# Kernel optimization log

Measured on AMD Instinct MI355X. Metric: run time of the kernel, lower is better.

Reference implementation:

```python
import jax, jax.numpy as jnp
import numpy as np

B, L, E, D = 4, 4096, 768, 64

def setup_inputs() -> dict:
    key = jax.random.key(0)
    ks = jax.random.split(key, 7)
    x = jax.random.normal(ks[0], (B, L, E), dtype=jnp.float32)
    # True = masked (strict upper triangle), as in masked_fill semantics
    causal_mask = jnp.triu(jnp.ones((L, L), dtype=bool), k=1)
    # True = valid token (inverted with ~ inside forward); all valid to avoid NaN rows
    pad_mask = jnp.ones((B, L), dtype=bool)
    s = 1.0 / np.sqrt(E)
    Wk = jax.random.uniform(ks[1], (E, D), jnp.float32, -s, s)
    bk = jax.random.uniform(ks[2], (D,), jnp.float32, -s, s)
    Wq = jax.random.uniform(ks[3], (E, D), jnp.float32, -s, s)
    bq = jax.random.uniform(ks[4], (D,), jnp.float32, -s, s)
    Wv = jax.random.uniform(ks[5], (E, D), jnp.float32, -s, s)
    bv = jax.random.uniform(ks[6], (D,), jnp.float32, -s, s)
    return {"x": x, "causal_mask": causal_mask, "pad_mask": pad_mask,
            "Wk": Wk, "bk": bk, "Wq": Wq, "bq": bq, "Wv": Wv, "bv": bv}

def reference(x, causal_mask, pad_mask, Wk, bk, Wq, bq, Wv, bv):
    # Linear projections: [B,L,E] @ [E,D] + [D]
    K = jnp.einsum('ble,ed->bld', x, Wk) + bk
    Q = jnp.einsum('ble,ed->bld', x, Wq) + bq
    V = jnp.einsum('ble,ed->bld', x, Wv) + bv
    d = Q.shape[-1]
    scores = jnp.einsum('bqd,bkd->bqk', Q, K) / jnp.sqrt(jnp.asarray(d, Q.dtype))
    # full_mask: causal (True=masked) OR key-position padding (~pad_mask, broadcast over query dim)
    full_mask = causal_mask[None, :, :] | (~pad_mask)[:, None, :]
    scores = jnp.where(full_mask, -jnp.inf, scores)
    attn = jax.nn.softmax(scores, axis=-1)
    out = jnp.einsum('bqk,bkd->bqd', attn, V)
    return out
```

## Files before the change

kernel.cpp:

```cpp
#include <hip/hip_runtime.h>

#define L_SEQ 4096
#define BATCH 4
#define EDIM 768

typedef __attribute__((ext_vector_type(8))) short bf16x8;
typedef __attribute__((ext_vector_type(4))) float f32x4;
typedef __attribute__((ext_vector_type(4))) unsigned short u16x4;
typedef __attribute__((ext_vector_type(8))) unsigned short u16x8;
typedef __attribute__((ext_vector_type(4))) _Float16 f16x4;
typedef __attribute__((ext_vector_type(8))) _Float16 f16x8;

__device__ __forceinline__ unsigned short f2bf(float f) {
  unsigned u = __builtin_bit_cast(unsigned, f);
  u += 0x7FFFu + ((u >> 16) & 1u);
  return (unsigned short)(u >> 16);
}

__global__ __launch_bounds__(256) void prep_kernel(
    const float* __restrict__ Wq, const float* __restrict__ Wk,
    const float* __restrict__ Wv, unsigned short* __restrict__ WT) {
  int g = blockIdx.x * 256 + threadIdx.x;
  if (g >= 192 * EDIM) return;
  int row = g / EDIM, k = g - row * EDIM;
  int z = row >> 6, n = row & 63;
  const float* W = (z == 0) ? Wq : (z == 1) ? Wk : Wv;
  WT[g] = f2bf(W[k * 64 + n]);
}

__global__ __launch_bounds__(256) void proj_kernel(
    const float* __restrict__ x, const unsigned short* __restrict__ WT,
    const float* __restrict__ bq, const float* __restrict__ bk, const float* __restrict__ bv,
    unsigned short* __restrict__ Qo, unsigned short* __restrict__ Kf,
    _Float16* __restrict__ Vf) {
  __shared__ unsigned short As[64 * 72];
  __shared__ unsigned short Bs[192 * 72];
  int tid = threadIdx.x;
  int w = tid >> 6, lane = tid & 63, l15 = lane & 15, g4 = lane >> 4;
  int m0 = blockIdx.x * 64;

  f32x4 acc[3][4];
#pragma unroll
  for (int z = 0; z < 3; z++)
#pragma unroll
    for (int cf = 0; cf < 4; cf++) acc[z][cf] = (f32x4){0.f, 0.f, 0.f, 0.f};

  int arow = tid >> 4, acs = tid & 15;
  int brow = tid >> 3, bsg = tid & 7;

  for (int k0 = 0; k0 < EDIM; k0 += 64) {
#pragma unroll
    for (int p = 0; p < 4; p++) {
      int row = arow + p * 16;
      f32x4 v = *(const f32x4*)(x + (size_t)(m0 + row) * EDIM + k0 + acs * 4);
      u16x4 sv;
      sv[0] = f2bf(v[0]); sv[1] = f2bf(v[1]); sv[2] = f2bf(v[2]); sv[3] = f2bf(v[3]);
      *(u16x4*)(&As[row * 72 + acs * 4]) = sv;
    }
#pragma unroll
    for (int p = 0; p < 6; p++) {
      int row = brow + p * 32;
      u16x8 v = *(const u16x8*)(WT + (size_t)row * EDIM + k0 + bsg * 8);
      *(u16x8*)(&Bs[row * 72 + bsg * 8]) = v;
    }
    __syncthreads();
#pragma unroll
    for (int ks = 0; ks < 64; ks += 32) {
      bf16x8 a = *(const bf16x8*)(&As[(16 * w + l15) * 72 + ks + g4 * 8]);
#pragma unroll
      for (int z = 0; z < 3; z++) {
#pragma unroll
        for (int cf = 0; cf < 4; cf++) {
          bf16x8 bb = *(const bf16x8*)(&Bs[(z * 64 + cf * 16 + l15) * 72 + ks + g4 * 8]);
          acc[z][cf] = __builtin_amdgcn_mfma_f32_16x16x32_bf16(a, bb, acc[z][cf], 0, 0, 0);
        }
      }
    }
    __syncthreads();
  }

#pragma unroll
  for (int cf = 0; cf < 4; cf++) {
    int col = cf * 16 + l15;
    float bqv = bq[col], bkv = bk[col], bvv = bv[col];
#pragma unroll
    for (int r = 0; r < 4; r++) {
      int row = m0 + 16 * w + g4 * 4 + r;
      Qo[(size_t)row * 64 + col] = f2bf((acc[0][cf][r] + bqv) * 0.125f);
      int b_ = row >> 12, l = row & 4095, j = l >> 6, t = l & 63;
      size_t blk = (size_t)(b_ * 64 + j) * 4096;
      size_t kidx = blk + (size_t)(((col >> 5) * 4 + (t >> 4)) * 512 +
                                   (((col >> 3) & 3) * 16 + (t & 15)) * 8 + (col & 7));
      Kf[kidx] = f2bf(acc[1][cf][r] + bkv);
      size_t vidx = blk + (size_t)(((t >> 4) * 2 + (col >> 5)) * 512 +
                                   ((((t >> 2) & 3) * 16) + (col & 15)) * 8 +
                                   ((col >> 4) & 1) * 4 + (t & 3));
      Vf[vidx] = (_Float16)(acc[2][cf][r] + bvv);
    }
  }
}

__global__ __launch_bounds__(256) void attn_kernel(
    const unsigned short* __restrict__ Qp, const unsigned short* __restrict__ Kf,
    const _Float16* __restrict__ Vf, float* __restrict__ out) {
  __shared__ float Ob[2][4][16][68];
  __shared__ float Ml[2][4][2][16];
  int tid = threadIdx.x;
  int p = tid >> 6, lane = tid & 63, l15 = lane & 15, g4 = lane >> 4;
  int flat = blockIdx.x;
  int xcd = flat & 7;
  int b = xcd >> 1;
  int pid = ((xcd & 1) << 6) + (flat >> 3);
  int sA = pid, sB = 255 - pid;
  size_t bL = (size_t)b * L_SEQ;

  float mA, lA; f32x4 oA[4];
  float mB, lB; f32x4 oB[4];

  auto run = [&](int s, f32x4 (&o)[4], float& m, float& l) {
    m = -1e38f; l = 0.f;
#pragma unroll
    for (int i = 0; i < 4; i++) o[i] = (f32x4){0.f, 0.f, 0.f, 0.f};
    int qrow = s * 16 + l15;
    const unsigned short* Qb = Qp + (bL + qrow) * 64 + g4 * 8;
    bf16x8 qf0 = *(const bf16x8*)Qb;
    bf16x8 qf1 = *(const bf16x8*)(Qb + 32);
    int jmax = s >> 2;
    for (int j = p; j <= jmax; j += 4) {
      const unsigned short* kb = Kf + (size_t)(b * 64 + j) * 4096 + lane * 8;
      const _Float16* vb = Vf + (size_t)(b * 64 + j) * 4096 + lane * 8;
      bf16x8 kf0[4], kf1[4];
#pragma unroll
      for (int tb = 0; tb < 4; tb++) kf0[tb] = *(const bf16x8*)(kb + tb * 512);
#pragma unroll
      for (int tb = 0; tb < 4; tb++) kf1[tb] = *(const bf16x8*)(kb + 2048 + tb * 512);
      f16x8 vp[8];
#pragma unroll
      for (int q = 0; q < 8; q++) vp[q] = *(const f16x8*)(vb + q * 512);

      f32x4 st[4];
#pragma unroll
      for (int tb = 0; tb < 4; tb++) st[tb] = (f32x4){0.f, 0.f, 0.f, 0.f};
#pragma unroll
      for (int tb = 0; tb < 4; tb++)
        st[tb] = __builtin_amdgcn_mfma_f32_16x16x32_bf16(kf0[tb], qf0, st[tb], 0, 0, 0);
#pragma unroll
      for (int tb = 0; tb < 4; tb++)
        st[tb] = __builtin_amdgcn_mfma_f32_16x16x32_bf16(kf1[tb], qf1, st[tb], 0, 0, 0);

      if (j == jmax) {
#pragma unroll
        for (int tb = 0; tb < 4; tb++)
#pragma unroll
          for (int r = 0; r < 4; r++)
            if (j * 64 + tb * 16 + g4 * 4 + r > qrow) st[tb][r] = -1e30f;
      }

      float mx = st[0][0];
#pragma unroll
      for (int tb = 0; tb < 4; tb++)
#pragma unroll
        for (int r = 0; r < 4; r++) mx = fmaxf(mx, st[tb][r]);
      mx = fmaxf(mx, __shfl_xor(mx, 16));
      mx = fmaxf(mx, __shfl_xor(mx, 32));
      float mn = fmaxf(m, mx);
      float scale = __expf(m - mn);
      m = mn;
      float rs = 0.f;
#pragma unroll
      for (int tb = 0; tb < 4; tb++)
#pragma unroll
        for (int r = 0; r < 4; r++) { st[tb][r] = __expf(st[tb][r] - mn); rs += st[tb][r]; }
      rs += __shfl_xor(rs, 16);
      rs += __shfl_xor(rs, 32);
      l = l * scale + rs;
#pragma unroll
      for (int cf = 0; cf < 4; cf++)
#pragma unroll
        for (int r = 0; r < 4; r++) o[cf][r] *= scale;

      f16x4 ph[4];
#pragma unroll
      for (int tb = 0; tb < 4; tb++) {
        ph[tb][0] = (_Float16)st[tb][0];
        ph[tb][1] = (_Float16)st[tb][1];
        ph[tb][2] = (_Float16)st[tb][2];
        ph[tb][3] = (_Float16)st[tb][3];
      }
#pragma unroll
      for (int tb = 0; tb < 4; tb++) {
#pragma unroll
        for (int cf = 0; cf < 4; cf++) {
          f16x8 pr = vp[tb * 2 + (cf >> 1)];
          f16x4 va = (cf & 1) ? (f16x4){pr[4], pr[5], pr[6], pr[7]}
                              : (f16x4){pr[0], pr[1], pr[2], pr[3]};
          o[cf] = __builtin_amdgcn_mfma_f32_16x16x16f16(va, ph[tb], o[cf], 0, 0, 0);
        }
      }
    }
  };

  run(sA, oA, mA, lA);
  run(sB, oB, mB, lB);

#pragma unroll
  for (int cf = 0; cf < 4; cf++) {
    *(f32x4*)&Ob[0][p][l15][cf * 16 + g4 * 4] = oA[cf];
    *(f32x4*)&Ob[1][p][l15][cf * 16 + g4 * 4] = oB[cf];
  }
  Ml[0][p][0][l15] = mA; Ml[0][p][1][l15] = lA;
  Ml[1][p][0][l15] = mB; Ml[1][p][1][l15] = lB;
  __syncthreads();

  if (p < 2) {
    int s = p ? sB : sA;
    int q = lane >> 2, ch = lane & 3;
    float mw[4], lw[4];
#pragma unroll
    for (int w = 0; w < 4; w++) { mw[w] = Ml[p][w][0][q]; lw[w] = Ml[p][w][1][q]; }
    float ms = fmaxf(fmaxf(mw[0], mw[1]), fmaxf(mw[2], mw[3]));
    float ew[4]; float denom = 0.f;
#pragma unroll
    for (int w = 0; w < 4; w++) { ew[w] = __expf(mw[w] - ms); denom += lw[w] * ew[w]; }
    float inv = 1.0f / denom;
#pragma unroll
    for (int i = 0; i < 4; i++) {
      f32x4 acc = (f32x4){0.f, 0.f, 0.f, 0.f};
#pragma unroll
      for (int w = 0; w < 4; w++) {
        f32x4 v = *(const f32x4*)&Ob[p][w][q][ch * 16 + i * 4];
        acc += v * ew[w];
      }
      acc *= inv;
      *(f32x4*)(out + (bL + s * 16 + q) * 64 + ch * 16 + i * 4) = acc;
    }
  }
}

extern "C" void kernel_launch(void* const* d_in, const int* in_sizes, int n_in,
                              void* d_out, int out_size, void* d_ws, size_t ws_size,
                              hipStream_t stream) {
  const float* x  = (const float*)d_in[0];
  const float* Wk = (const float*)d_in[3];
  const float* bk = (const float*)d_in[4];
  const float* Wq = (const float*)d_in[5];
  const float* bq = (const float*)d_in[6];
  const float* Wv = (const float*)d_in[7];
  const float* bv = (const float*)d_in[8];
  float* out = (float*)d_out;

  char* ws = (char*)d_ws;
  unsigned short* WT = (unsigned short*)ws;
  unsigned short* Qo = (unsigned short*)(ws + 294912);
  unsigned short* Kf = (unsigned short*)(ws + 294912 + 2097152);
  _Float16*       Vf = (_Float16*)(ws + 294912 + 2 * 2097152);

  prep_kernel<<<576, 256, 0, stream>>>(Wq, Wk, Wv, WT);
  proj_kernel<<<256, 256, 0, stream>>>(x, WT, bq, bk, bv, Qo, Kf, Vf);
  attn_kernel<<<512, 256, 0, stream>>>(Qo, Kf, Vf, out);
}
```

Before: 55.86 us.

## Software-pipeline projection and attention loads; stage outputs through LDS; lazy rescale

The projection kernel now double-buffers its weight tiles in shared memory and register-prefetches the next x and W slices while computing the current one. It builds A fragments directly from registers, skipping the LDS round trip for x. Outputs are staged in LDS and written out with coalesced 16-byte stores instead of scattered 2-byte stores. The attention kernel double-buffers K/V register loads across iterations, raises wave priority around MFMA blocks, and skips the online-softmax rescale unless the running max grows by more than a threshold. The cost is higher register pressure, which may reduce occupancy.

```diff
diff --git a/kernel.cpp b/kernel.cpp
--- a/kernel.cpp
+++ b/kernel.cpp
@@ -33,11 +33,11 @@
     const float* __restrict__ bq, const float* __restrict__ bk, const float* __restrict__ bv,
     unsigned short* __restrict__ Qo, unsigned short* __restrict__ Kf,
     _Float16* __restrict__ Vf) {
-  __shared__ unsigned short As[64 * 72];
-  __shared__ unsigned short Bs[192 * 72];
+  __shared__ unsigned short SH[2 * 13824];
   int tid = threadIdx.x;
   int w = tid >> 6, lane = tid & 63, l15 = lane & 15, g4 = lane >> 4;
   int m0 = blockIdx.x * 64;
+  int brow = tid >> 3, bsg = tid & 7;
 
   f32x4 acc[3][4];
 #pragma unroll
@@ -45,58 +45,97 @@
 #pragma unroll
     for (int cf = 0; cf < 4; cf++) acc[z][cf] = (f32x4){0.f, 0.f, 0.f, 0.f};
 
-  int arow = tid >> 4, acs = tid & 15;
-  int brow = tid >> 3, bsg = tid & 7;
-
-  for (int k0 = 0; k0 < EDIM; k0 += 64) {
-#pragma unroll
-    for (int p = 0; p < 4; p++) {
-      int row = arow + p * 16;
-      f32x4 v = *(const f32x4*)(x + (size_t)(m0 + row) * EDIM + k0 + acs * 4);
-      u16x4 sv;
-      sv[0] = f2bf(v[0]); sv[1] = f2bf(v[1]); sv[2] = f2bf(v[2]); sv[3] = f2bf(v[3]);
-      *(u16x4*)(&As[row * 72 + acs * 4]) = sv;
-    }
-#pragma unroll
-    for (int p = 0; p < 6; p++) {
-      int row = brow + p * 32;
-      u16x8 v = *(const u16x8*)(WT + (size_t)row * EDIM + k0 + bsg * 8);
-      *(u16x8*)(&Bs[row * 72 + bsg * 8]) = v;
-    }
-    __syncthreads();
-#pragma unroll
-    for (int ks = 0; ks < 64; ks += 32) {
-      bf16x8 a = *(const bf16x8*)(&As[(16 * w + l15) * 72 + ks + g4 * 8]);
-#pragma unroll
-      for (int z = 0; z < 3; z++) {
+  f32x4 arA[4], arB[4];
+  u16x8 brA[6], brB[6];
+
+  auto loadA = [&](f32x4 (&ar)[4], int k0) {
+    const float* xp = x + (size_t)(m0 + 16 * w + l15) * EDIM + k0 + g4 * 8;
+    ar[0] = *(const f32x4*)xp;
+    ar[1] = *(const f32x4*)(xp + 4);
+    ar[2] = *(const f32x4*)(xp + 32);
+    ar[3] = *(const f32x4*)(xp + 36);
+  };
+  auto loadB = [&](u16x8 (&br)[6], int k0) {
+#pragma unroll
+    for (int pp = 0; pp < 6; pp++)
+      br[pp] = *(const u16x8*)(WT + (size_t)(brow + pp * 32) * EDIM + k0 + bsg * 8);
+  };
+  auto writeB = [&](int cur, u16x8 (&br)[6]) {
+#pragma unroll
+    for (int pp = 0; pp < 6; pp++)
+      *(u16x8*)&SH[cur * 13824 + (brow + pp * 32) * 72 + bsg * 8] = br[pp];
+  };
+  auto mkfrag = [&](f32x4 lo, f32x4 hi) {
+    union { u16x8 u; bf16x8 b; } r;
+    r.u[0] = f2bf(lo[0]); r.u[1] = f2bf(lo[1]); r.u[2] = f2bf(lo[2]); r.u[3] = f2bf(lo[3]);
+    r.u[4] = f2bf(hi[0]); r.u[5] = f2bf(hi[1]); r.u[6] = f2bf(hi[2]); r.u[7] = f2bf(hi[3]);
+    return r.b;
+  };
+  auto compute = [&](int cur, f32x4 (&ar)[4]) {
+#pragma unroll
+    for (int ks = 0; ks < 2; ks++) {
+      bf16x8 a = mkfrag(ar[ks * 2], ar[ks * 2 + 1]);
+#pragma unroll
+      for (int z = 0; z < 3; z++)
 #pragma unroll
         for (int cf = 0; cf < 4; cf++) {
-          bf16x8 bb = *(const bf16x8*)(&Bs[(z * 64 + cf * 16 + l15) * 72 + ks + g4 * 8]);
+          bf16x8 bb = *(const bf16x8*)&SH[cur * 13824 + (z * 64 + cf * 16 + l15) * 72 +
+                                          ks * 32 + g4 * 8];
           acc[z][cf] = __builtin_amdgcn_mfma_f32_16x16x32_bf16(a, bb, acc[z][cf], 0, 0, 0);
         }
-      }
-    }
+    }
+  };
+
+  loadA(arA, 0);
+  loadB(brA, 0);
+  for (int ss = 0; ss < 6; ss++) {
+    int k1 = (2 * ss + 1) * 64;
+    loadA(arB, k1);
+    loadB(brB, k1);
+    writeB(0, brA);
     __syncthreads();
+    compute(0, arA);
+    if (ss < 5) {
+      int k2 = (2 * ss + 2) * 64;
+      loadA(arA, k2);
+      loadB(brA, k2);
+    }
+    writeB(1, brB);
+    __syncthreads();
+    compute(1, arB);
   }
 
+  __syncthreads();
 #pragma unroll
   for (int cf = 0; cf < 4; cf++) {
     int col = cf * 16 + l15;
     float bqv = bq[col], bkv = bk[col], bvv = bv[col];
 #pragma unroll
     for (int r = 0; r < 4; r++) {
-      int row = m0 + 16 * w + g4 * 4 + r;
-      Qo[(size_t)row * 64 + col] = f2bf((acc[0][cf][r] + bqv) * 0.125f);
-      int b_ = row >> 12, l = row & 4095, j = l >> 6, t = l & 63;
-      size_t blk = (size_t)(b_ * 64 + j) * 4096;
-      size_t kidx = blk + (size_t)(((col >> 5) * 4 + (t >> 4)) * 512 +
-                                   (((col >> 3) & 3) * 16 + (t & 15)) * 8 + (col & 7));
-      Kf[kidx] = f2bf(acc[1][cf][r] + bkv);
-      size_t vidx = blk + (size_t)(((t >> 4) * 2 + (col >> 5)) * 512 +
-                                   ((((t >> 2) & 3) * 16) + (col & 15)) * 8 +
-                                   ((col >> 4) & 1) * 4 + (t & 3));
-      Vf[vidx] = (_Float16)(acc[2][cf][r] + bvv);
-    }
+      int t = 16 * w + g4 * 4 + r;
+      SH[t * 64 + col] = f2bf((acc[0][cf][r] + bqv) * 0.125f);
+      int kidx = ((col >> 5) * 4 + (t >> 4)) * 512 +
+                 (((col >> 3) & 3) * 16 + (t & 15)) * 8 + (col & 7);
+      SH[4096 + kidx] = f2bf(acc[1][cf][r] + bkv);
+      int vidx = ((t >> 4) * 2 + (col >> 5)) * 512 +
+                 ((((t >> 2) & 3) * 16) + (col & 15)) * 8 + ((col >> 4) & 1) * 4 + (t & 3);
+      _Float16 hv = (_Float16)(acc[2][cf][r] + bvv);
+      SH[8192 + vidx] = *(unsigned short*)&hv;
+    }
+  }
+  __syncthreads();
+  {
+    int b_ = m0 >> 12, jj = (m0 >> 6) & 63;
+    size_t blk = (size_t)(b_ * 64 + jj) * 4096;
+    const u16x8* s0 = (const u16x8*)&SH[tid * 16];
+    u16x8* dq = (u16x8*)(Qo + (size_t)m0 * 64 + tid * 16);
+    dq[0] = s0[0]; dq[1] = s0[1];
+    const u16x8* s1 = (const u16x8*)&SH[4096 + tid * 16];
+    u16x8* dk = (u16x8*)(Kf + blk + tid * 16);
+    dk[0] = s1[0]; dk[1] = s1[1];
+    const u16x8* s2 = (const u16x8*)&SH[8192 + tid * 16];
+    u16x8* dv = (u16x8*)((unsigned short*)Vf + blk + tid * 16);
+    dv[0] = s2[0]; dv[1] = s2[1];
   }
 }
 
@@ -114,102 +153,131 @@
   int sA = pid, sB = 255 - pid;
   size_t bL = (size_t)b * L_SEQ;
 
-  float mA, lA; f32x4 oA[4];
-  float mB, lB; f32x4 oB[4];
-
-  auto run = [&](int s, f32x4 (&o)[4], float& m, float& l) {
+  const unsigned short* Kb = Kf + (size_t)b * 64 * 4096;
+  const _Float16* Vb = Vf + (size_t)b * 64 * 4096;
+
+  f32x4 o[4];
+  float m, l;
+  bf16x8 qf0, qf1;
+  int qrow, jmax;
+
+  auto loadkv = [&](bf16x8 (&kf)[8], f16x8 (&vp)[8], int j) {
+    const unsigned short* kb = Kb + (size_t)j * 4096 + lane * 8;
+    const _Float16* vb = Vb + (size_t)j * 4096 + lane * 8;
+#pragma unroll
+    for (int q = 0; q < 8; q++) kf[q] = *(const bf16x8*)(kb + q * 512);
+#pragma unroll
+    for (int q = 0; q < 8; q++) vp[q] = *(const f16x8*)(vb + q * 512);
+  };
+
+  auto step = [&](bf16x8 (&kf)[8], f16x8 (&vp)[8], int j) {
+    f32x4 st[4];
+#pragma unroll
+    for (int i = 0; i < 4; i++) st[i] = (f32x4){0.f, 0.f, 0.f, 0.f};
+    __builtin_amdgcn_s_setprio(1);
+#pragma unroll
+    for (int tb = 0; tb < 4; tb++)
+      st[tb] = __builtin_amdgcn_mfma_f32_16x16x32_bf16(kf[tb], qf0, st[tb], 0, 0, 0);
+#pragma unroll
+    for (int tb = 0; tb < 4; tb++)
+      st[tb] = __builtin_amdgcn_mfma_f32_16x16x32_bf16(kf[4 + tb], qf1, st[tb], 0, 0, 0);
+    __builtin_amdgcn_s_setprio(0);
+
+    if (j == jmax) {
+#pragma unroll
+      for (int tb = 0; tb < 4; tb++)
+#pragma unroll
+        for (int r = 0; r < 4; r++)
+          if (j * 64 + tb * 16 + g4 * 4 + r > qrow) st[tb][r] = -1e30f;
+    }
+
+    float mx = st[0][0];
+#pragma unroll
+    for (int tb = 0; tb < 4; tb++)
+#pragma unroll
+      for (int r = 0; r < 4; r++) mx = fmaxf(mx, st[tb][r]);
+    mx = fmaxf(mx, __shfl_xor(mx, 16));
+    mx = fmaxf(mx, __shfl_xor(mx, 32));
+    if (!__all(mx <= m + 8.0f)) {
+      float mn = fmaxf(m, mx);
+      float sc = __expf(m - mn);
+      m = mn;
+      l *= sc;
+#pragma unroll
+      for (int cf = 0; cf < 4; cf++)
+#pragma unroll
+        for (int r = 0; r < 4; r++) o[cf][r] *= sc;
+    }
+    float rs = 0.f;
+#pragma unroll
+    for (int tb = 0; tb < 4; tb++)
+#pragma unroll
+      for (int r = 0; r < 4; r++) { st[tb][r] = __expf(st[tb][r] - m); rs += st[tb][r]; }
+    rs += __shfl_xor(rs, 16);
+    rs += __shfl_xor(rs, 32);
+    l += rs;
+
+    f16x4 ph[4];
+#pragma unroll
+    for (int tb = 0; tb < 4; tb++) {
+      ph[tb][0] = (_Float16)st[tb][0]; ph[tb][1] = (_Float16)st[tb][1];
+      ph[tb][2] = (_Float16)st[tb][2]; ph[tb][3] = (_Float16)st[tb][3];
+    }
+    __builtin_amdgcn_s_setprio(1);
+#pragma unroll
+    for (int tb = 0; tb < 4; tb++) {
+#pragma unroll
+      for (int cf = 0; cf < 4; cf++) {
+        f16x8 pr = vp[tb * 2 + (cf >> 1)];
+        f16x4 va = (cf & 1) ? (f16x4){pr[4], pr[5], pr[6], pr[7]}
+                            : (f16x4){pr[0], pr[1], pr[2], pr[3]};
+        o[cf] = __builtin_amdgcn_mfma_f32_16x16x16f16(va, ph[tb], o[cf], 0, 0, 0);
+      }
+    }
+    __builtin_amdgcn_s_setprio(0);
+  };
+
+  bf16x8 kfA[8], kfB[8];
+  f16x8 vpA[8], vpB[8];
+
+  auto run = [&](int s) {
     m = -1e38f; l = 0.f;
 #pragma unroll
     for (int i = 0; i < 4; i++) o[i] = (f32x4){0.f, 0.f, 0.f, 0.f};
-    int qrow = s * 16 + l15;
+    qrow = s * 16 + l15;
+    jmax = s >> 2;
     const unsigned short* Qb = Qp + (bL + qrow) * 64 + g4 * 8;
-    bf16x8 qf0 = *(const bf16x8*)Qb;
-    bf16x8 qf1 = *(const bf16x8*)(Qb + 32);
-    int jmax = s >> 2;
-    for (int j = p; j <= jmax; j += 4) {
-      const unsigned short* kb = Kf + (size_t)(b * 64 + j) * 4096 + lane * 8;
-      const _Float16* vb = Vf + (size_t)(b * 64 + j) * 4096 + lane * 8;
-      bf16x8 kf0[4], kf1[4];
-#pragma unroll
-      for (int tb = 0; tb < 4; tb++) kf0[tb] = *(const bf16x8*)(kb + tb * 512);
-#pragma unroll
-      for (int tb = 0; tb < 4; tb++) kf1[tb] = *(const bf16x8*)(kb + 2048 + tb * 512);
-      f16x8 vp[8];
-#pragma unroll
-      for (int q = 0; q < 8; q++) vp[q] = *(const f16x8*)(vb + q * 512);
-
-      f32x4 st[4];
-#pragma unroll
-      for (int tb = 0; tb < 4; tb++) st[tb] = (f32x4){0.f, 0.f, 0.f, 0.f};
-#pragma unroll
-      for (int tb = 0; tb < 4; tb++)
-        st[tb] = __builtin_amdgcn_mfma_f32_16x16x32_bf16(kf0[tb], qf0, st[tb], 0, 0, 0);
-#pragma unroll
-      for (int tb = 0; tb < 4; tb++)
-        st[tb] = __builtin_amdgcn_mfma_f32_16x16x32_bf16(kf1[tb], qf1, st[tb], 0, 0, 0);
-
-      if (j == jmax) {
-#pragma unroll
-        for (int tb = 0; tb < 4; tb++)
-#pragma unroll
-          for (int r = 0; r < 4; r++)
-            if (j * 64 + tb * 16 + g4 * 4 + r > qrow) st[tb][r] = -1e30f;
-      }
-
-      float mx = st[0][0];
-#pragma unroll
-      for (int tb = 0; tb < 4; tb++)
-#pragma unroll
-        for (int r = 0; r < 4; r++) mx = fmaxf(mx, st[tb][r]);
-      mx = fmaxf(mx, __shfl_xor(mx, 16));
-      mx = fmaxf(mx, __shfl_xor(mx, 32));
-      float mn = fmaxf(m, mx);
-      float scale = __expf(m - mn);
-      m = mn;
-      float rs = 0.f;
-#pragma unroll
-      for (int tb = 0; tb < 4; tb++)
-#pragma unroll
-        for (int r = 0; r < 4; r++) { st[tb][r] = __expf(st[tb][r] - mn); rs += st[tb][r]; }
-      rs += __shfl_xor(rs, 16);
-      rs += __shfl_xor(rs, 32);
-      l = l * scale + rs;
-#pragma unroll
-      for (int cf = 0; cf < 4; cf++)
-#pragma unroll
-        for (int r = 0; r < 4; r++) o[cf][r] *= scale;
-
-      f16x4 ph[4];
-#pragma unroll
-      for (int tb = 0; tb < 4; tb++) {
-        ph[tb][0] = (_Float16)st[tb][0];
-        ph[tb][1] = (_Float16)st[tb][1];
-        ph[tb][2] = (_Float16)st[tb][2];
-        ph[tb][3] = (_Float16)st[tb][3];
-      }
-#pragma unroll
-      for (int tb = 0; tb < 4; tb++) {
-#pragma unroll
-        for (int cf = 0; cf < 4; cf++) {
-          f16x8 pr = vp[tb * 2 + (cf >> 1)];
-          f16x4 va = (cf & 1) ? (f16x4){pr[4], pr[5], pr[6], pr[7]}
-                              : (f16x4){pr[0], pr[1], pr[2], pr[3]};
-          o[cf] = __builtin_amdgcn_mfma_f32_16x16x16f16(va, ph[tb], o[cf], 0, 0, 0);
-        }
-      }
-    }
-  };
-
-  run(sA, oA, mA, lA);
-  run(sB, oB, mB, lB);
-
-#pragma unroll
-  for (int cf = 0; cf < 4; cf++) {
-    *(f32x4*)&Ob[0][p][l15][cf * 16 + g4 * 4] = oA[cf];
-    *(f32x4*)&Ob[1][p][l15][cf * 16 + g4 * 4] = oB[cf];
-  }
-  Ml[0][p][0][l15] = mA; Ml[0][p][1][l15] = lA;
-  Ml[1][p][0][l15] = mB; Ml[1][p][1][l15] = lB;
+    qf0 = *(const bf16x8*)Qb;
+    qf1 = *(const bf16x8*)(Qb + 32);
+    int j = p;
+    if (j > jmax) return;
+    loadkv(kfA, vpA, j);
+    while (true) {
+      int jn = j + 4;
+      bool hasB = (jn <= jmax);
+      if (hasB) loadkv(kfB, vpB, jn);
+      step(kfA, vpA, j);
+      if (!hasB) break;
+      j = jn;
+      jn = j + 4;
+      bool hasA = (jn <= jmax);
+      if (hasA) loadkv(kfA, vpA, jn);
+      step(kfB, vpB, j);
+      if (!hasA) break;
+      j = jn;
+    }
+  };
+
+  auto stash = [&](int side) {
+#pragma unroll
+    for (int cf = 0; cf < 4; cf++)
+      *(f32x4*)&Ob[side][p][l15][cf * 16 + g4 * 4] = o[cf];
+    Ml[side][p][0][l15] = m;
+    Ml[side][p][1][l15] = l;
+  };
+
+  run(sA); stash(0);
+  run(sB); stash(1);
   __syncthreads();
 
   if (p < 2) {
```

Measured after the change: 53.89 us. -3.5%, faster.
